# Optimization experiments

Hardware: AMD Instinct MI355X
Metric: run time of the kernel (lower is better)

The kernel has to match this reference:

```python
import jax, jax.numpy as jnp
from jax import lax
import numpy as np

N, T, PD, TD, F, E, GB = 2048, 256, 5, 5, 128, 65536, 5


def _lstm_layer(x, Wih, Whh, bih, bhh):
    # x: [B, T, D] -> [B, T, H], torch LSTM gate order (i, f, g, o)
    B = x.shape[0]
    H = Whh.shape[1]
    b = bih + bhh

    def step(carry, xt):
        h, c = carry
        gates = xt @ Wih.T + h @ Whh.T + b
        i, f, g, o = jnp.split(gates, 4, axis=-1)
        c = jax.nn.sigmoid(f) * c + jax.nn.sigmoid(i) * jnp.tanh(g)
        h = jax.nn.sigmoid(o) * jnp.tanh(c)
        return (h, c), h

    h0 = jnp.zeros((B, H), x.dtype)
    _, hs = lax.scan(step, (h0, h0), jnp.swapaxes(x, 0, 1))
    return jnp.swapaxes(hs, 0, 1)


def _attention(x, W1, b1, W2, b2):
    # Fused prefix (cumulative causal) softmax attention.
    # Original loops over t computing softmax(scores[:, :t+1]); here:
    # ctx[t] = cumsum(e * x)[t] / cumsum(e)[t] with a global max shift
    # (softmax is shift-invariant, so this equals the per-prefix softmax).
    s = (jnp.tanh(x @ W1.T + b1) @ W2.T + b2)[..., 0]  # [B, T]
    e = jnp.exp(s - jnp.max(s, axis=1, keepdims=True))  # [B, T]
    num = jnp.cumsum(e[..., None] * x, axis=1)          # [B, T, D]
    den = jnp.cumsum(e, axis=1)[..., None]              # [B, T, 1]
    return jnp.sum(num / den, axis=1)                   # [B, D]


def _gcn(x, W, b, edge_index, edge_weight):
    # PyG GCNConv with normalize=True: add self-loops (w=1), symmetric norm.
    n = x.shape[0]
    loop = jnp.arange(n)
    row = jnp.concatenate([edge_index[0], loop])
    col = jnp.concatenate([edge_index[1], loop])
    w = jnp.concatenate([edge_weight, jnp.ones((n,), edge_weight.dtype)])
    deg = jax.ops.segment_sum(w, col, num_segments=n)
    dinv = jnp.where(deg > 0, deg ** -0.5, 0.0)
    norm = dinv[row] * w * dinv[col]
    h = x @ W.T
    out = jax.ops.segment_sum(norm[:, None] * h[row], col, num_segments=n)
    return out + b


def _forward(price, global_trend, p_weights, t_weights,
             lp_Wih0, lp_Whh0, lp_bih0, lp_bhh0, lp_Wih1, lp_Whh1, lp_bih1, lp_bhh1,
             lt_Wih0, lt_Whh0, lt_bih0, lt_bhh0, lt_Wih1, lt_Whh1, lt_bih1, lt_bhh1,
             ap_W1, ap_b1, ap_W2, ap_b2, at_W1, at_b1, at_W2, at_b2,
             gp1_W, gp1_b, gp2_W, gp2_b, gt1_W, gt1_b, gt2_W, gt2_b,
             mlp_W, mlp_b, p_edge_index, t_edge_index):
    x = _lstm_layer(price, lp_Wih0, lp_Whh0, lp_bih0, lp_bhh0)
    x = _lstm_layer(x, lp_Wih1, lp_Whh1, lp_bih1, lp_bhh1)
    x = _attention(x, ap_W1, ap_b1, ap_W2, ap_b2)            # [N, F]
    g = _lstm_layer(global_trend, lt_Wih0, lt_Whh0, lt_bih0, lt_bhh0)
    g = _lstm_layer(g, lt_Wih1, lt_Whh1, lt_bih1, lt_bhh1)
    g = _attention(g, at_W1, at_b1, at_W2, at_b2)            # [GB, F]
    pg = _gcn(x, gp1_W, gp1_b, p_edge_index, p_weights)
    pg = _gcn(pg, gp2_W, gp2_b, p_edge_index, p_weights)     # [N, F]
    # NOTE: original feeds x (not g) into the trend graph convs.
    tg = _gcn(x, gt1_W, gt1_b, t_edge_index, t_weights)
    tg = _gcn(tg, gt2_W, gt2_b, t_edge_index, t_weights)     # [N, F]
    trend = tg @ g.T                                         # [N, GB]
    feat = jnp.concatenate([pg, trend], axis=1)              # [N, F+GB]
    return jax.nn.sigmoid(feat @ mlp_W.T + mlp_b)            # [N, 1]


def setup_inputs() -> dict:
    key = jax.random.key(0)
    ks = iter(jax.random.split(key, 64))
    nrm = lambda shape, s=0.05: jax.random.normal(next(ks), shape, jnp.float32) * s
    inp = {}
    inp['price'] = jax.random.normal(next(ks), (N, T, PD), jnp.float32)
    inp['global_trend'] = jax.random.normal(next(ks), (GB, T, TD), jnp.float32)
    inp['p_edge_index'] = jax.random.randint(next(ks), (2, E), 0, N)
    inp['p_weights'] = jax.random.uniform(next(ks), (E,), jnp.float32)
    inp['t_edge_index'] = jax.random.randint(next(ks), (2, E), 0, N)
    inp['t_weights'] = jax.random.uniform(next(ks), (E,), jnp.float32)
    for pre, d in (('lp', PD), ('lt', TD)):
        inp[pre + '_Wih0'] = nrm((4 * F, d)); inp[pre + '_Whh0'] = nrm((4 * F, F))
        inp[pre + '_bih0'] = nrm((4 * F,));   inp[pre + '_bhh0'] = nrm((4 * F,))
        inp[pre + '_Wih1'] = nrm((4 * F, F)); inp[pre + '_Whh1'] = nrm((4 * F, F))
        inp[pre + '_bih1'] = nrm((4 * F,));   inp[pre + '_bhh1'] = nrm((4 * F,))
    for pre in ('ap', 'at'):
        inp[pre + '_W1'] = nrm((F, F)); inp[pre + '_b1'] = jnp.zeros((F,), jnp.float32)
        inp[pre + '_W2'] = nrm((1, F)); inp[pre + '_b2'] = jnp.zeros((1,), jnp.float32)
    for pre in ('gp', 'gt'):
        inp[pre + '1_W'] = nrm((16, F)); inp[pre + '1_b'] = jnp.zeros((16,), jnp.float32)
        inp[pre + '2_W'] = nrm((F, 16)); inp[pre + '2_b'] = jnp.zeros((F,), jnp.float32)
    inp['mlp_W'] = nrm((1, F + GB)); inp['mlp_b'] = jnp.zeros((1,), jnp.float32)
    return inp


def reference(price, global_trend, p_edge_index, p_weights, t_edge_index, t_weights,
              lp_Wih0, lp_Whh0, lp_bih0, lp_bhh0, lp_Wih1, lp_Whh1, lp_bih1, lp_bhh1,
              lt_Wih0, lt_Whh0, lt_bih0, lt_bhh0, lt_Wih1, lt_Whh1, lt_bih1, lt_bhh1,
              ap_W1, ap_b1, ap_W2, ap_b2, at_W1, at_b1, at_W2, at_b2,
              gp1_W, gp1_b, gp2_W, gp2_b, gt1_W, gt1_b, gt2_W, gt2_b,
              mlp_W, mlp_b):
    return _forward(price, global_trend, p_weights, t_weights,
                    lp_Wih0, lp_Whh0, lp_bih0, lp_bhh0, lp_Wih1, lp_Whh1, lp_bih1, lp_bhh1,
                    lt_Wih0, lt_Whh0, lt_bih0, lt_bhh0, lt_Wih1, lt_Whh1, lt_bih1, lt_bhh1,
                    ap_W1, ap_b1, ap_W2, ap_b2, at_W1, at_b1, at_W2, at_b2,
                    gp1_W, gp1_b, gp2_W, gp2_b, gt1_W, gt1_b, gt2_W, gt2_b,
                    mlp_W, mlp_b, p_edge_index, t_edge_index)
```

## Files before the change

### kernel.cpp

```cpp
#include <hip/hip_runtime.h>
#include <hip/hip_bf16.h>
#include <cstddef>

#define TT    256
#define NROW  2048
#define GBN   5
#define EDG   65536

using f32x4  = __attribute__((ext_vector_type(4))) float;
using bf16x8 = __attribute__((ext_vector_type(8))) short;

__device__ __forceinline__ void pinv(bf16x8& x) { asm volatile("" : "+v"(x)); }

__device__ __forceinline__ void barrier_lgkm() {
  asm volatile("s_waitcnt lgkmcnt(0)" ::: "memory");
  __builtin_amdgcn_s_barrier();
}

__device__ __forceinline__ float exp2fa(float x) { float r; asm("v_exp_f32 %0, %1" : "=v"(r) : "v"(x)); return r; }
__device__ __forceinline__ float rcpfa(float x)  { float r; asm("v_rcp_f32 %0, %1" : "=v"(r) : "v"(x)); return r; }
#define L2E 1.4426950408889634f
__device__ __forceinline__ float sigf(float x) { return rcpfa(1.0f + exp2fa(x * -L2E)); }
__device__ __forceinline__ float tanh_fast(float x) {
  float t = exp2fa(x * (-2.0f * L2E));
  return (1.0f - t) * rcpfa(1.0f + t);
}

enum : int {
  XBUF   = 425984,
  GBUFO  = 688128,
  DINVP  = 688768,
  DINVT  = 690816,
  H16    = 692864,
  PG1    = 725632,
  H128   = 758400,
  PGB    = 1020544,
  TG1    = 1282688,
  TGB    = 1315456,
  WS_END = 1577600
};

enum : int {
  N_P0   = 0,
  N_P1I  = 65536,
  N_P1H  = 131072,
  N_PA   = 196608,
  N_T0   = 212992,
  N_T1I  = 278528,
  N_T1H  = 344064,
  N_TA   = 409600
};

enum : long long {
  C0S_O   = 1577600,
  C1S_O   = 1843840,
  H1IMG_O = 2108032,
  SMST_O  = 2372224,
  NUMS_O  = 2376352,
  ACCOS_O = 2640544,
  H0S_O   = 2904736
};

struct __align__(16) SmemPipe {
  ushort a[2][4096];
  ushort b[2][4096];
  float  x[5120];
  float  s[2][8][16];
  float  pad[8192];
};

__global__ void k_pack(const float* __restrict__ Wa, const float* __restrict__ Wb,
                       int K1, int K2, int NT, int KS, ushort* __restrict__ dst) {
  int t = blockIdx.x * blockDim.x + threadIdx.x;
  int total = KS * NT * 2 * 64;
  if (t >= total) return;
  int lane = t & 63;
  int part = (t >> 6) & 1;
  int rest = t >> 7;
  int nt = rest % NT, kk = rest / NT;
  int j = nt * 16 + (lane & 15);
  int kbase = kk * 32 + (lane >> 4) * 8;
  bf16x8 o;
  #pragma unroll
  for (int e = 0; e < 8; ++e) {
    int k = kbase + e;
    float x = (k < K1) ? Wa[(size_t)j * K1 + k] : Wb[(size_t)j * K2 + (k - K1)];
    __hip_bfloat16 hi = __float2bfloat16(x);
    ushort u;
    if (part == 0) {
      u = *(ushort*)&hi;
    } else {
      float lo = x - __bfloat162float(hi);
      __hip_bfloat16 lob = __float2bfloat16(lo);
      u = *(ushort*)&lob;
    }
    o[e] = (short)u;
  }
  ((bf16x8*)dst)[t] = o;
}

__global__ void k_zero(float* __restrict__ p, int n) {
  int i = blockIdx.x * blockDim.x + threadIdx.x;
  if (i < n) p[i] = 0.0f;
}
__global__ void k_fill1(float* __restrict__ p, int n) {
  int i = blockIdx.x * blockDim.x + threadIdx.x;
  if (i < n) p[i] = 1.0f;
}
__global__ void k_deg(const int* __restrict__ col, const float* __restrict__ w,
                      float* __restrict__ deg, int n) {
  int i = blockIdx.x * blockDim.x + threadIdx.x;
  if (i < n) atomicAdd(&deg[col[i]], w[i]);
}
__global__ void k_dinv(float* __restrict__ deg, int n) {
  int i = blockIdx.x * blockDim.x + threadIdx.x;
  if (i < n) deg[i] = rsqrtf(deg[i]);
}

__device__ static void lstm0_body(
    SmemPipe* sm, int b,
    const float* __restrict__ price, const float* __restrict__ gtrend,
    const float* __restrict__ ws_ro, ushort* __restrict__ h0S, float* __restrict__ c0S,
    const float* __restrict__ Wih0p, const float* __restrict__ bi0p, const float* __restrict__ bh0p,
    const float* __restrict__ Wih0t, const float* __restrict__ bi0t, const float* __restrict__ bh0t,
    int nP32, int t0, int TCp, int first)
{
  const int tid = threadIdx.x;
  const int w = tid >> 6, l = tid & 63;
  const int lq = l >> 4, lr = l & 15;
  const int rb = lq * 4;
  const int kcol = w * 16 + lr;
  const bool isP = b < nP32;
  const int R = isP ? 32 : GBN;
  const float* seq = isP ? (price + (size_t)b * 32 * (TT * 5)) : gtrend;
  const ushort* S0 = (const ushort*)(ws_ro + (isP ? N_P0 : N_T0));
  const float* Wih0 = isP ? Wih0p : Wih0t;
  const float* bi0 = isP ? bi0p : bi0t;
  const float* bh0 = isP ? bh0p : bh0t;

  auto h0hi = sm->a;
  auto h0lo = sm->b;
  float* xsa = sm->x;

  bf16x8 wh[4][4], wl[4][4];
  #pragma unroll
  for (int kk = 0; kk < 4; ++kk)
    #pragma unroll
    for (int g = 0; g < 4; ++g) {
      int blk = (kk * 32 + (w + 8 * g)) * 2;
      wh[kk][g] = ((const bf16x8*)S0)[(blk + 0) * 64 + l];
      wl[kk][g] = ((const bf16x8*)S0)[(blk + 1) * 64 + l];
      pinv(wh[kk][g]); pinv(wl[kk][g]);
    }
  float wih0r[4][5], bg0[4];
  #pragma unroll
  for (int g = 0; g < 4; ++g) {
    int j = kcol + 128 * g;
    bg0[g] = bi0[j] + bh0[j];
    #pragma unroll
    for (int k = 0; k < 5; ++k) wih0r[g][k] = Wih0[j * 5 + k];
  }

  const size_t bstr = (size_t)b * (size_t)TCp * 8192;
  float c0[2][4] = {{0, 0, 0, 0}, {0, 0, 0, 0}};

  for (int i = tid; i < TCp * 160; i += 512) {
    int tl = i / 160, rem = i % 160, r = rem / 5, k = rem % 5;
    xsa[tl * 160 + rem] = (r < R) ? seq[(size_t)r * (TT * 5) + (size_t)(t0 + tl) * 5 + k] : 0.0f;
  }
  if (first) {
    for (int i = tid; i < 4096; i += 512) { h0hi[0][i] = 0; h0lo[0][i] = 0; }
  } else {
    const size_t lb = bstr + (size_t)(TCp - 1) * 8192;
    *(uint4*)&h0hi[0][8 * tid] = *(const uint4*)&h0S[lb + 8 * tid];
    *(uint4*)&h0lo[0][8 * tid] = *(const uint4*)&h0S[lb + 4096 + 8 * tid];
    #pragma unroll
    for (int t = 0; t < 2; ++t)
      #pragma unroll
      for (int reg = 0; reg < 4; ++reg)
        c0[t][reg] = c0S[(size_t)b * 4096 + (size_t)(t * 16 + rb + reg) * 128 + kcol];
  }
  __syncthreads();

  const int kkhi = (kcol >> 3) & 3;
  const int eo = kcol & 7;
  const int b0w = rb + 16 * kkhi;
  const int kkw = kcol >> 5;
  int wro[4];
  #pragma unroll
  for (int reg = 0; reg < 4; ++reg) wro[reg] = kkw * 512 + (b0w + (reg ^ lq)) * 8 + eo;
  const int rdo = (l ^ ((l >> 2) & 3)) * 8;

  int cur = 0;
  for (int tl = 0; tl < TCp; ++tl) {
    const int nxt = cur ^ 1;
    if (tl > 0) {
      *(uint4*)&h0S[bstr + (size_t)(tl - 1) * 8192 + 8 * tid] = *(const uint4*)&h0hi[cur][8 * tid];
      *(uint4*)&h0S[bstr + (size_t)(tl - 1) * 8192 + 4096 + 8 * tid] = *(const uint4*)&h0lo[cur][8 * tid];
    }

    f32x4 acc[2][4];
    #pragma unroll
    for (int t = 0; t < 2; ++t)
      #pragma unroll
      for (int g = 0; g < 4; ++g) acc[t][g] = (f32x4){bg0[g], bg0[g], bg0[g], bg0[g]};
    #pragma unroll
    for (int k = 0; k < 5; ++k) {
      float xv[2][4];
      #pragma unroll
      for (int t = 0; t < 2; ++t)
        #pragma unroll
        for (int reg = 0; reg < 4; ++reg)
          xv[t][reg] = xsa[tl * 160 + (t * 16 + rb + reg) * 5 + k];
      #pragma unroll
      for (int t = 0; t < 2; ++t)
        #pragma unroll
        for (int g = 0; g < 4; ++g)
          #pragma unroll
          for (int reg = 0; reg < 4; ++reg)
            acc[t][g][reg] = fmaf(xv[t][reg], wih0r[g][k], acc[t][g][reg]);
    }
    #pragma unroll
    for (int kk = 0; kk < 4; ++kk) {
      bf16x8 ah0 = *(const bf16x8*)&h0hi[cur][kk * 512 + rdo];
      bf16x8 al0 = *(const bf16x8*)&h0lo[cur][kk * 512 + rdo];
      bf16x8 ah1 = *(const bf16x8*)&h0hi[cur][2048 + kk * 512 + rdo];
      bf16x8 al1 = *(const bf16x8*)&h0lo[cur][2048 + kk * 512 + rdo];
      #pragma unroll
      for (int g = 0; g < 4; ++g) {
        acc[0][g] = __builtin_amdgcn_mfma_f32_16x16x32_bf16(ah0, wh[kk][g], acc[0][g], 0, 0, 0);
        acc[0][g] = __builtin_amdgcn_mfma_f32_16x16x32_bf16(al0, wh[kk][g], acc[0][g], 0, 0, 0);
        acc[0][g] = __builtin_amdgcn_mfma_f32_16x16x32_bf16(ah0, wl[kk][g], acc[0][g], 0, 0, 0);
        acc[1][g] = __builtin_amdgcn_mfma_f32_16x16x32_bf16(ah1, wh[kk][g], acc[1][g], 0, 0, 0);
        acc[1][g] = __builtin_amdgcn_mfma_f32_16x16x32_bf16(al1, wh[kk][g], acc[1][g], 0, 0, 0);
        acc[1][g] = __builtin_amdgcn_mfma_f32_16x16x32_bf16(ah1, wl[kk][g], acc[1][g], 0, 0, 0);
      }
    }
    #pragma unroll
    for (int t = 0; t < 2; ++t)
      #pragma unroll
      for (int reg = 0; reg < 4; ++reg) {
        float gi = acc[0 + t][0][reg], gf = acc[t][1][reg], gg = acc[t][2][reg], go = acc[t][3][reg];
        float c = sigf(gf) * c0[t][reg] + sigf(gi) * tanh_fast(gg);
        c0[t][reg] = c;
        float h = sigf(go) * tanh_fast(c);
        __hip_bfloat16 hb = __float2bfloat16(h);
        float lo = h - __bfloat162float(hb);
        __hip_bfloat16 lb = __float2bfloat16(lo);
        h0hi[nxt][t * 2048 + wro[reg]] = *(ushort*)&hb;
        h0lo[nxt][t * 2048 + wro[reg]] = *(ushort*)&lb;
      }
    barrier_lgkm();
    cur = nxt;
  }
  *(uint4*)&h0S[bstr + (size_t)(TCp - 1) * 8192 + 8 * tid] = *(const uint4*)&h0hi[cur][8 * tid];
  *(uint4*)&h0S[bstr + (size_t)(TCp - 1) * 8192 + 4096 + 8 * tid] = *(const uint4*)&h0lo[cur][8 * tid];

  #pragma unroll
  for (int t = 0; t < 2; ++t)
    #pragma unroll
    for (int reg = 0; reg < 4; ++reg)
      c0S[(size_t)b * 4096 + (size_t)(t * 16 + rb + reg) * 128 + kcol] = c0[t][reg];
}

__device__ static void lstm1_body(
    SmemPipe* sm, int b,
    const float* __restrict__ pre1, const float* __restrict__ ws_ro,
    float* __restrict__ xout, float* __restrict__ gout,
    float* __restrict__ c1S, ushort* __restrict__ h1imgS, float* __restrict__ smS,
    float* __restrict__ numS, float* __restrict__ accOS,
    const float* __restrict__ apB1, const float* __restrict__ apW2, const float* __restrict__ apB2,
    const float* __restrict__ atB1, const float* __restrict__ atW2, const float* __restrict__ atB2,
    int nPrice, int TCp, int first)
{
  const int tid = threadIdx.x;
  const int w = tid >> 6, l = tid & 63;
  const int lq = l >> 4, lr = l & 15;
  const int rb = lq * 4;
  const int kcol = w * 16 + lr;
  const bool isP = b < nPrice;
  const int R = isP ? 16 : GBN;
  const ushort* S1H = (const ushort*)(ws_ro + (isP ? N_P1H : N_T1H));
  const ushort* SA  = (const ushort*)(ws_ro + (isP ? N_PA : N_TA));
  const float* b1ap = isP ? apB1 : atB1;
  const float* w2p  = isP ? apW2 : atW2;
  const float  b2v  = isP ? apB2[0] : atB2[0];

  auto h1hi = sm->a;
  auto h1lo = sm->b;
  auto sbuf = sm->s;

  bf16x8 hh[4][4], hl[4][4];
  #pragma unroll
  for (int kk = 0; kk < 4; ++kk)
    #pragma unroll
    for (int g = 0; g < 4; ++g) {
      int blk = (kk * 32 + (w + 8 * g)) * 2;
      hh[kk][g] = ((const bf16x8*)S1H)[(blk + 0) * 64 + l];
      hl[kk][g] = ((const bf16x8*)S1H)[(blk + 1) * 64 + l];
      pinv(hh[kk][g]); pinv(hl[kk][g]);
    }
  bf16x8 wa[4], wal[4];
  #pragma unroll
  for (int kk = 0; kk < 4; ++kk) {
    wa[kk]  = ((const bf16x8*)SA)[((kk * 8 + w) * 2 + 0) * 64 + l];
    wal[kk] = ((const bf16x8*)SA)[((kk * 8 + w) * 2 + 1) * 64 + l];
    pinv(wa[kk]); pinv(wal[kk]);
  }
  const float w2r = w2p[kcol], b1ar = b1ap[kcol];

  float c1[4] = {0, 0, 0, 0}, h1r[4] = {0, 0, 0, 0}, h1r_prev[4];
  float num[4] = {0, 0, 0, 0}, accO[4] = {0, 0, 0, 0};
  float m_run[4], den_r[4];

  if (first) {
    for (int i = tid; i < 2048; i += 512) { h1hi[0][i] = 0; h1lo[0][i] = 0; }
    #pragma unroll
    for (int reg = 0; reg < 4; ++reg) { m_run[reg] = -1e30f; den_r[reg] = 0.0f; }
  } else {
    const size_t ib = (size_t)b * 4096;
    *(uint2*)&h1hi[0][4 * tid] = *(const uint2*)&h1imgS[ib + 4 * tid];
    *(uint2*)&h1lo[0][4 * tid] = *(const uint2*)&h1imgS[ib + 2048 + 4 * tid];
    const size_t sb = (size_t)b * 2048;
    #pragma unroll
    for (int reg = 0; reg < 4; ++reg) {
      size_t o = sb + (size_t)(rb + reg) * 128 + kcol;
      c1[reg] = c1S[o];
      num[reg] = numS[o];
      accO[reg] = accOS[o];
      m_run[reg] = smS[(size_t)b * 32 + (size_t)(rb + reg) * 2];
      den_r[reg] = smS[(size_t)b * 32 + (size_t)(rb + reg) * 2 + 1];
    }
  }
  __syncthreads();

  const int kkhi = (kcol >> 3) & 3;
  const int eo = kcol & 7;
  const int b0w = rb + 16 * kkhi;
  const int kkw = kcol >> 5;
  int wro[4];
  #pragma unroll
  for (int reg = 0; reg < 4; ++reg) wro[reg] = kkw * 512 + (b0w + (reg ^ lq)) * 8 + eo;
  const int rdo = (l ^ ((l >> 2) & 3)) * 8;

  const float* pbase = pre1 + (size_t)b * TCp * 8192 + (size_t)tid * 16;

  f32x4 pnext[4];
  #pragma unroll
  for (int g = 0; g < 4; ++g) pnext[g] = *(const f32x4*)&pbase[g * 4];

  int cur = 0;
  for (int tl = 0; tl < TCp; ++tl) {
    const int nxt = cur ^ 1;
    f32x4 acc[4];
    #pragma unroll
    for (int g = 0; g < 4; ++g) acc[g] = pnext[g];
    if (tl + 1 < TCp) {
      #pragma unroll
      for (int g = 0; g < 4; ++g)
        pnext[g] = *(const f32x4*)&pbase[(size_t)(tl + 1) * 8192 + g * 4];
    }

    #pragma unroll
    for (int kk = 0; kk < 4; ++kk) {
      bf16x8 ah = *(const bf16x8*)&h1hi[cur][kk * 512 + rdo];
      bf16x8 al = *(const bf16x8*)&h1lo[cur][kk * 512 + rdo];
      #pragma unroll
      for (int g = 0; g < 4; ++g) {
        acc[g] = __builtin_amdgcn_mfma_f32_16x16x32_bf16(ah, hh[kk][g], acc[g], 0, 0, 0);
        acc[g] = __builtin_amdgcn_mfma_f32_16x16x32_bf16(al, hh[kk][g], acc[g], 0, 0, 0);
        acc[g] = __builtin_amdgcn_mfma_f32_16x16x32_bf16(ah, hl[kk][g], acc[g], 0, 0, 0);
      }
    }
    #pragma unroll
    for (int reg = 0; reg < 4; ++reg) {
      h1r_prev[reg] = h1r[reg];
      float gi = acc[0][reg], gf = acc[1][reg], gg = acc[2][reg], go = acc[3][reg];
      float c = sigf(gf) * c1[reg] + sigf(gi) * tanh_fast(gg);
      c1[reg] = c;
      float h = sigf(go) * tanh_fast(c);
      h1r[reg] = h;
      __hip_bfloat16 hb = __float2bfloat16(h);
      float lo = h - __bfloat162float(hb);
      __hip_bfloat16 lb = __float2bfloat16(lo);
      h1hi[nxt][wro[reg]] = *(ushort*)&hb;
      h1lo[nxt][wro[reg]] = *(ushort*)&lb;
    }
    barrier_lgkm();

    if (tl > 0) {
      const int pb = (tl - 1) & 1;
      #pragma unroll
      for (int reg = 0; reg < 4; ++reg) {
        float s = b2v;
        #pragma unroll
        for (int ww = 0; ww < 8; ++ww) s += sbuf[pb][ww][rb + reg];
        float m0 = m_run[reg];
        float nm = fmaxf(m0, s);
        float e = exp2fa((s - nm) * L2E), sc = exp2fa((m0 - nm) * L2E);
        float d = den_r[reg] * sc + e;
        m_run[reg] = nm; den_r[reg] = d;
        num[reg] = num[reg] * sc + e * h1r_prev[reg];
        accO[reg] = fmaf(num[reg], rcpfa(d), accO[reg]);
      }
    }

    f32x4 aa = (f32x4){b1ar, b1ar, b1ar, b1ar};
    #pragma unroll
    for (int kk = 0; kk < 4; ++kk) {
      bf16x8 ah = *(const bf16x8*)&h1hi[nxt][kk * 512 + rdo];
      bf16x8 al = *(const bf16x8*)&h1lo[nxt][kk * 512 + rdo];
      aa = __builtin_amdgcn_mfma_f32_16x16x32_bf16(ah, wa[kk], aa, 0, 0, 0);
      aa = __builtin_amdgcn_mfma_f32_16x16x32_bf16(al, wa[kk], aa, 0, 0, 0);
      aa = __builtin_amdgcn_mfma_f32_16x16x32_bf16(ah, wal[kk], aa, 0, 0, 0);
    }
    float p[4];
    #pragma unroll
    for (int reg = 0; reg < 4; ++reg) p[reg] = tanh_fast(aa[reg]) * w2r;
    #pragma unroll
    for (int m = 1; m < 16; m <<= 1) {
      #pragma unroll
      for (int reg = 0; reg < 4; ++reg) p[reg] += __shfl_xor(p[reg], m);
    }
    if (lr == 0) {
      #pragma unroll
      for (int reg = 0; reg < 4; ++reg) sbuf[tl & 1][w][rb + reg] = p[reg];
    }
    cur = nxt;
  }
  barrier_lgkm();
  {
    const int pb = (TCp - 1) & 1;
    #pragma unroll
    for (int reg = 0; reg < 4; ++reg) {
      float s = b2v;
      #pragma unroll
      for (int ww = 0; ww < 8; ++ww) s += sbuf[pb][ww][rb + reg];
      float m0 = m_run[reg];
      float nm = fmaxf(m0, s);
      float e = exp2fa((s - nm) * L2E), sc = exp2fa((m0 - nm) * L2E);
      float d = den_r[reg] * sc + e;
      m_run[reg] = nm; den_r[reg] = d;
      num[reg] = num[reg] * sc + e * h1r[reg];
      accO[reg] = fmaf(num[reg], rcpfa(d), accO[reg]);
    }
  }

  {
    const size_t ib = (size_t)b * 4096;
    *(uint2*)&h1imgS[ib + 4 * tid] = *(const uint2*)&h1hi[cur][4 * tid];
    *(uint2*)&h1imgS[ib + 2048 + 4 * tid] = *(const uint2*)&h1lo[cur][4 * tid];
    const size_t sb = (size_t)b * 2048;
    #pragma unroll
    for (int reg = 0; reg < 4; ++reg) {
      size_t o = sb + (size_t)(rb + reg) * 128 + kcol;
      c1S[o] = c1[reg];
      numS[o] = num[reg];
      accOS[o] = accO[reg];
    }
    if (w == 0 && lr == 0) {
      #pragma unroll
      for (int reg = 0; reg < 4; ++reg) {
        smS[(size_t)b * 32 + (size_t)(rb + reg) * 2] = m_run[reg];
        smS[(size_t)b * 32 + (size_t)(rb + reg) * 2 + 1] = den_r[reg];
      }
    }
  }

  float* dstx = isP ? (xout + (size_t)b * 16 * 128) : gout;
  #pragma unroll
  for (int reg = 0; reg < 4; ++reg) {
    int r = rb + reg;
    if (r < R) dstx[(size_t)r * 128 + kcol] = accO[reg];
  }
}

__global__ __launch_bounds__(512, 2) void k_pipe(
    const float* __restrict__ price, const float* __restrict__ gtrend,
    const float* __restrict__ ws_ro, ushort* __restrict__ h0S, float* __restrict__ c0S,
    const float* __restrict__ Wih0p, const float* __restrict__ bi0p, const float* __restrict__ bh0p,
    const float* __restrict__ Wih0t, const float* __restrict__ bi0t, const float* __restrict__ bh0t,
    const float* __restrict__ pre1,
    float* __restrict__ xout, float* __restrict__ gout,
    float* __restrict__ c1S, ushort* __restrict__ h1imgS, float* __restrict__ smS,
    float* __restrict__ numS, float* __restrict__ accOS,
    const float* __restrict__ apB1, const float* __restrict__ apW2, const float* __restrict__ apB2,
    const float* __restrict__ atB1, const float* __restrict__ atW2, const float* __restrict__ atB2,
    int t0A, int TCp, int firstA, int firstB, int doA, int doB)
{
  __shared__ SmemPipe sm;
  const int bid = blockIdx.x;
  if (bid < 65) {
    if (doA)
      lstm0_body(&sm, bid, price, gtrend, ws_ro, h0S, c0S,
                 Wih0p, bi0p, bh0p, Wih0t, bi0t, bh0t, 64, t0A, TCp, firstA);
  } else {
    if (doB)
      lstm1_body(&sm, bid - 65, pre1, ws_ro, xout, gout,
                 c1S, h1imgS, smS, numS, accOS,
                 apB1, apW2, apB2, atB1, atW2, atB2, 128, TCp, firstB);
  }
}

__global__ __launch_bounds__(512, 2) void k_pre1(
    const ushort* __restrict__ h0S, const float* __restrict__ ws_ro,
    float* __restrict__ pre1,
    const float* __restrict__ bi1p, const float* __restrict__ bh1p,
    const float* __restrict__ bi1t, const float* __restrict__ bh1t,
    int nPrice, int TCp, int nsub)
{
  const int b16 = blockIdx.x / nsub, sub = blockIdx.x % nsub;
  const int b32 = b16 >> 1, tile = b16 & 1;
  const int tid = threadIdx.x;
  const int w = tid >> 6, l = tid & 63;
  const int lr = l & 15;
  const int kcol = w * 16 + lr;
  const bool isP = b16 < nPrice;
  const ushort* S1I = (const ushort*)(ws_ro + (isP ? N_P1I : N_T1I));
  const float* bi1 = isP ? bi1p : bi1t;
  const float* bh1 = isP ? bh1p : bh1t;
  float bg1[4];
  #pragma unroll
  for (int g = 0; g < 4; ++g) bg1[g] = bi1[kcol + 128 * g] + bh1[kcol + 128 * g];
  const int rdo = (l ^ ((l >> 2) & 3)) * 8;
  const size_t bstr = (size_t)b32 * (size_t)TCp * 8192;
  const int t0 = sub * 4;

  f32x4 acc[4][4];
  #pragma unroll
  for (int ts = 0; ts < 4; ++ts)
    #pragma unroll
    for (int g = 0; g < 4; ++g) acc[ts][g] = (f32x4){bg1[g], bg1[g], bg1[g], bg1[g]};

  #pragma unroll
  for (int kk = 0; kk < 4; ++kk) {
    bf16x8 bh_[4], bl_[4];
    #pragma unroll
    for (int g = 0; g < 4; ++g) {
      int blk = (kk * 32 + (w + 8 * g)) * 2;
      bh_[g] = ((const bf16x8*)S1I)[(blk + 0) * 64 + l];
      bl_[g] = ((const bf16x8*)S1I)[(blk + 1) * 64 + l];
    }
    #pragma unroll
    for (int ts = 0; ts < 4; ++ts) {
      const size_t tb = bstr + (size_t)(t0 + ts) * 8192 + tile * 2048 + kk * 512 + rdo;
      bf16x8 ah = *(const bf16x8*)&h0S[tb];
      bf16x8 al = *(const bf16x8*)&h0S[tb + 4096];
      #pragma unroll
      for (int g = 0; g < 4; ++g) {
        acc[ts][g] = __builtin_amdgcn_mfma_f32_16x16x32_bf16(ah, bh_[g], acc[ts][g], 0, 0, 0);
        acc[ts][g] = __builtin_amdgcn_mfma_f32_16x16x32_bf16(al, bh_[g], acc[ts][g], 0, 0, 0);
        acc[ts][g] = __builtin_amdgcn_mfma_f32_16x16x32_bf16(ah, bl_[g], acc[ts][g], 0, 0, 0);
      }
    }
  }
  #pragma unroll
  for (int ts = 0; ts < 4; ++ts)
    #pragma unroll
    for (int g = 0; g < 4; ++g)
      *(f32x4*)&pre1[((size_t)b16 * TCp + (t0 + ts)) * 8192 + (size_t)tid * 16 + g * 4] = acc[ts][g];
}

__global__ void k_lin(const float* __restrict__ x, const float* __restrict__ W,
                      float* __restrict__ h, int M, int K, int n) {
  int i = blockIdx.x * blockDim.x + threadIdx.x;
  if (i >= n) return;
  int r = i / M, m = i % M;
  const float* xr = x + (size_t)r * K;
  const float* wm = W + (size_t)m * K;
  float a = 0.f;
  for (int k = 0; k < K; ++k) a = fmaf(xr[k], wm[k], a);
  h[i] = a;
}

__global__ void k_scatter(const int* __restrict__ rowi, const int* __restrict__ coli,
                          const float* __restrict__ w, const float* __restrict__ dinv,
                          const float* __restrict__ h, float* __restrict__ outp,
                          int M, long long n) {
  long long i = (long long)blockIdx.x * blockDim.x + threadIdx.x;
  if (i >= n) return;
  int e = (int)(i / M), f = (int)(i % M);
  int rs = rowi[e], cd = coli[e];
  float nrm = dinv[rs] * w[e] * dinv[cd];
  atomicAdd(&outp[(size_t)cd * M + f], nrm * h[(size_t)rs * M + f]);
}

__global__ void k_gcn_fin(float* __restrict__ io, const float* __restrict__ h,
                          const float* __restrict__ dinv, const float* __restrict__ b,
                          int M, int n) {
  int i = blockIdx.x * blockDim.x + threadIdx.x;
  if (i >= n) return;
  int v = i / M, f = i % M;
  float dv = dinv[v];
  io[i] += dv * dv * h[i] + b[f];
}

__global__ __launch_bounds__(256) void k_final(const float* __restrict__ pg, const float* __restrict__ tg,
                                               const float* __restrict__ g, const float* __restrict__ mw,
                                               const float* __restrict__ mb, float* __restrict__ outp) {
  int wv = threadIdx.x >> 6, ln = threadIdx.x & 63;
  int r = blockIdx.x * 4 + wv;
  const float* pr = pg + (size_t)r * 128;
  const float* tr = tg + (size_t)r * 128;
  float pa = pr[ln] * mw[ln] + pr[ln + 64] * mw[ln + 64];
  float t0 = tr[ln], t1 = tr[ln + 64];
  float s[GBN];
  #pragma unroll
  for (int gb = 0; gb < GBN; ++gb)
    s[gb] = g[gb * 128 + ln] * t0 + g[gb * 128 + 64 + ln] * t1;
  #pragma unroll
  for (int o = 32; o > 0; o >>= 1) {
    pa += __shfl_down(pa, o);
    #pragma unroll
    for (int gb = 0; gb < GBN; ++gb) s[gb] += __shfl_down(s[gb], o);
  }
  if (ln == 0) {
    float lg = pa + mb[0];
    #pragma unroll
    for (int gb = 0; gb < GBN; ++gb) lg = fmaf(s[gb], mw[128 + gb], lg);
    outp[r] = 1.0f / (1.0f + __expf(-lg));
  }
}

static inline int gdiv(long long n) { return (int)((n + 255) / 256); }

extern "C" void kernel_launch(void* const* d_in, const int* in_sizes, int n_in,
                              void* d_out, int out_size, void* d_ws, size_t ws_size,
                              hipStream_t stream) {
  const float* price  = (const float*)d_in[0];
  const float* gtrend = (const float*)d_in[1];
  const int*   p_ei   = (const int*)d_in[2];
  const float* p_w    = (const float*)d_in[3];
  const int*   t_ei   = (const int*)d_in[4];
  const float* t_w    = (const float*)d_in[5];
  const float* lpWih0 = (const float*)d_in[6];
  const float* lpWhh0 = (const float*)d_in[7];
  const float* lpBih0 = (const float*)d_in[8];
  const float* lpBhh0 = (const float*)d_in[9];
  const float* lpWih1 = (const float*)d_in[10];
  const float* lpWhh1 = (const float*)d_in[11];
  const float* lpBih1 = (const float*)d_in[12];
  const float* lpBhh1 = (const float*)d_in[13];
  const float* ltWih0 = (const float*)d_in[14];
  const float* ltWhh0 = (const float*)d_in[15];
  const float* ltBih0 = (const float*)d_in[16];
  const float* ltBhh0 = (const float*)d_in[17];
  const float* ltWih1 = (const float*)d_in[18];
  const float* ltWhh1 = (const float*)d_in[19];
  const float* ltBih1 = (const float*)d_in[20];
  const float* ltBhh1 = (const float*)d_in[21];
  const float* apW1 = (const float*)d_in[22];
  const float* apB1 = (const float*)d_in[23];
  const float* apW2 = (const float*)d_in[24];
  const float* apB2 = (const float*)d_in[25];
  const float* atW1 = (const float*)d_in[26];
  const float* atB1 = (const float*)d_in[27];
  const float* atW2 = (const float*)d_in[28];
  const float* atB2 = (const float*)d_in[29];
  const float* gp1W = (const float*)d_in[30];
  const float* gp1b = (const float*)d_in[31];
  const float* gp2W = (const float*)d_in[32];
  const float* gp2b = (const float*)d_in[33];
  const float* gt1W = (const float*)d_in[34];
  const float* gt1b = (const float*)d_in[35];
  const float* gt2W = (const float*)d_in[36];
  const float* gt2b = (const float*)d_in[37];
  const float* mlpW = (const float*)d_in[38];
  const float* mlpb = (const float*)d_in[39];

  float* ws = (float*)d_ws;
  float* outp = (float*)d_out;
  if (ws_size < (size_t)WS_END * sizeof(float)) return;

  int TC = 0;
  for (int cand = 32; cand >= 8; cand >>= 1) {
    unsigned long long need = ((unsigned long long)H0S_O +
                               65ULL * cand * 4096ULL + 129ULL * cand * 8192ULL) * 4ULL;
    if ((unsigned long long)ws_size >= need) { TC = cand; break; }
  }
  if (TC == 0) return;

  k_pack<<<gdiv(16384), 256, 0, stream>>>(lpWhh0, lpWhh0, 128, 128, 32, 4, (ushort*)(ws + N_P0));
  k_pack<<<gdiv(16384), 256, 0, stream>>>(lpWih1, lpWih1, 128, 128, 32, 4, (ushort*)(ws + N_P1I));
  k_pack<<<gdiv(16384), 256, 0, stream>>>(lpWhh1, lpWhh1, 128, 128, 32, 4, (ushort*)(ws + N_P1H));
  k_pack<<<gdiv(4096),  256, 0, stream>>>(apW1,   apW1,   128, 128,  8, 4, (ushort*)(ws + N_PA));
  k_pack<<<gdiv(16384), 256, 0, stream>>>(ltWhh0, ltWhh0, 128, 128, 32, 4, (ushort*)(ws + N_T0));
  k_pack<<<gdiv(16384), 256, 0, stream>>>(ltWih1, ltWih1, 128, 128, 32, 4, (ushort*)(ws + N_T1I));
  k_pack<<<gdiv(16384), 256, 0, stream>>>(ltWhh1, ltWhh1, 128, 128, 32, 4, (ushort*)(ws + N_T1H));
  k_pack<<<gdiv(4096),  256, 0, stream>>>(atW1,   atW1,   128, 128,  8, 4, (ushort*)(ws + N_TA));

  k_fill1<<<gdiv(NROW), 256, 0, stream>>>(ws + DINVP, NROW);
  k_deg<<<gdiv(EDG), 256, 0, stream>>>(p_ei + EDG, p_w, ws + DINVP, EDG);
  k_dinv<<<gdiv(NROW), 256, 0, stream>>>(ws + DINVP, NROW);
  k_fill1<<<gdiv(NROW), 256, 0, stream>>>(ws + DINVT, NROW);
  k_deg<<<gdiv(EDG), 256, 0, stream>>>(t_ei + EDG, t_w, ws + DINVT, EDG);
  k_dinv<<<gdiv(NROW), 256, 0, stream>>>(ws + DINVT, NROW);

  ushort* h0S = (ushort*)(ws + H0S_O);
  float*  pre1 = ws + H0S_O + (long long)65 * TC * 4096;
  {
    const int CH = TT / TC;
    const int nsub = TC / 4;
    for (int c = 0; c < CH; ++c) {
      k_pipe<<<194, 512, 0, stream>>>(price, gtrend, ws, h0S, ws + C0S_O,
                                      lpWih0, lpBih0, lpBhh0,
                                      ltWih0, ltBih0, ltBhh0,
                                      pre1, ws + XBUF, ws + GBUFO,
                                      ws + C1S_O, (ushort*)(ws + H1IMG_O), ws + SMST_O,
                                      ws + NUMS_O, ws + ACCOS_O,
                                      apB1, apW2, apB2, atB1, atW2, atB2,
                                      c * TC, TC,
                                      c == 0 ? 1 : 0, c == 1 ? 1 : 0,
                                      1, c > 0 ? 1 : 0);
      k_pre1<<<129 * nsub, 512, 0, stream>>>(h0S, ws, pre1,
                                             lpBih1, lpBhh1, ltBih1, ltBhh1,
                                             128, TC, nsub);
    }
    k_pipe<<<194, 512, 0, stream>>>(price, gtrend, ws, h0S, ws + C0S_O,
                                    lpWih0, lpBih0, lpBhh0,
                                    ltWih0, ltBih0, ltBhh0,
                                    pre1, ws + XBUF, ws + GBUFO,
                                    ws + C1S_O, (ushort*)(ws + H1IMG_O), ws + SMST_O,
                                    ws + NUMS_O, ws + ACCOS_O,
                                    apB1, apW2, apB2, atB1, atW2, atB2,
                                    0, TC, 0, CH == 1 ? 1 : 0, 0, 1);
  }

  k_lin<<<gdiv(NROW * 16), 256, 0, stream>>>(ws + XBUF, gp1W, ws + H16, 16, 128, NROW * 16);
  k_zero<<<gdiv(NROW * 16), 256, 0, stream>>>(ws + PG1, NROW * 16);
  k_scatter<<<gdiv((long long)EDG * 16), 256, 0, stream>>>(p_ei, p_ei + EDG, p_w, ws + DINVP,
                                                           ws + H16, ws + PG1, 16, (long long)EDG * 16);
  k_gcn_fin<<<gdiv(NROW * 16), 256, 0, stream>>>(ws + PG1, ws + H16, ws + DINVP, gp1b, 16, NROW * 16);
  k_lin<<<gdiv(NROW * 128), 256, 0, stream>>>(ws + PG1, gp2W, ws + H128, 128, 16, NROW * 128);
  k_zero<<<gdiv(NROW * 128), 256, 0, stream>>>(ws + PGB, NROW * 128);
  k_scatter<<<gdiv((long long)EDG * 128), 256, 0, stream>>>(p_ei, p_ei + EDG, p_w, ws + DINVP,
                                                            ws + H128, ws + PGB, 128, (long long)EDG * 128);
  k_gcn_fin<<<gdiv(NROW * 128), 256, 0, stream>>>(ws + PGB, ws + H128, ws + DINVP, gp2b, 128, NROW * 128);

  k_lin<<<gdiv(NROW * 16), 256, 0, stream>>>(ws + XBUF, gt1W, ws + H16, 16, 128, NROW * 16);
  k_zero<<<gdiv(NROW * 16), 256, 0, stream>>>(ws + TG1, NROW * 16);
  k_scatter<<<gdiv((long long)EDG * 16), 256, 0, stream>>>(t_ei, t_ei + EDG, t_w, ws + DINVT,
                                                           ws + H16, ws + TG1, 16, (long long)EDG * 16);
  k_gcn_fin<<<gdiv(NROW * 16), 256, 0, stream>>>(ws + TG1, ws + H16, ws + DINVT, gt1b, 16, NROW * 16);
  k_lin<<<gdiv(NROW * 128), 256, 0, stream>>>(ws + TG1, gt2W, ws + H128, 128, 16, NROW * 128);
  k_zero<<<gdiv(NROW * 128), 256, 0, stream>>>(ws + TGB, NROW * 128);
  k_scatter<<<gdiv((long long)EDG * 128), 256, 0, stream>>>(t_ei, t_ei + EDG, t_w, ws + DINVT,
                                                            ws + H128, ws + TGB, 128, (long long)EDG * 128);
  k_gcn_fin<<<gdiv(NROW * 128), 256, 0, stream>>>(ws + TGB, ws + H128, ws + DINVT, gt2b, 128, NROW * 128);

  k_final<<<512, 256, 0, stream>>>(ws + PGB, ws + TGB, ws + GBUFO, mlpW, mlpb, outp);
}
```

Before: 2.426 ms.

## Fuse layer-1 input projection into pipelined LSTM kernel with double-buffered h0

Removes the separate k_pre1 launch per chunk. Each layer-1 block now computes its own input projection (pre1) from the previous chunk's layer-0 hidden states at the start of k_pipe. To make this safe while layer-0 blocks write the current chunk, the h0 staging buffer is double-buffered (ping-pong hA/hB), which doubles its workspace footprint. This cuts kernel launches and lets the projection overlap with layer-0 recurrence, but it adds serial work at the front of each layer-1 block.

```diff
diff --git a/kernel.cpp b/kernel.cpp
--- a/kernel.cpp
+++ b/kernel.cpp
@@ -120,17 +120,18 @@
 __device__ static void lstm0_body(
     SmemPipe* sm, int b,
     const float* __restrict__ price, const float* __restrict__ gtrend,
-    const float* __restrict__ ws_ro, ushort* __restrict__ h0S, float* __restrict__ c0S,
+    const float* __restrict__ ws_ro, ushort* __restrict__ h0W,
+    const ushort* __restrict__ h0R, float* __restrict__ c0S,
     const float* __restrict__ Wih0p, const float* __restrict__ bi0p, const float* __restrict__ bh0p,
     const float* __restrict__ Wih0t, const float* __restrict__ bi0t, const float* __restrict__ bh0t,
-    int nP32, int t0, int TCp, int first)
+    int t0, int TCp, int first)
 {
   const int tid = threadIdx.x;
   const int w = tid >> 6, l = tid & 63;
   const int lq = l >> 4, lr = l & 15;
   const int rb = lq * 4;
   const int kcol = w * 16 + lr;
-  const bool isP = b < nP32;
+  const bool isP = b < 64;
   const int R = isP ? 32 : GBN;
   const float* seq = isP ? (price + (size_t)b * 32 * (TT * 5)) : gtrend;
   const ushort* S0 = (const ushort*)(ws_ro + (isP ? N_P0 : N_T0));
@@ -172,8 +173,8 @@
     for (int i = tid; i < 4096; i += 512) { h0hi[0][i] = 0; h0lo[0][i] = 0; }
   } else {
     const size_t lb = bstr + (size_t)(TCp - 1) * 8192;
-    *(uint4*)&h0hi[0][8 * tid] = *(const uint4*)&h0S[lb + 8 * tid];
-    *(uint4*)&h0lo[0][8 * tid] = *(const uint4*)&h0S[lb + 4096 + 8 * tid];
+    *(uint4*)&h0hi[0][8 * tid] = *(const uint4*)&h0R[lb + 8 * tid];
+    *(uint4*)&h0lo[0][8 * tid] = *(const uint4*)&h0R[lb + 4096 + 8 * tid];
     #pragma unroll
     for (int t = 0; t < 2; ++t)
       #pragma unroll
@@ -195,8 +196,8 @@
   for (int tl = 0; tl < TCp; ++tl) {
     const int nxt = cur ^ 1;
     if (tl > 0) {
-      *(uint4*)&h0S[bstr + (size_t)(tl - 1) * 8192 + 8 * tid] = *(const uint4*)&h0hi[cur][8 * tid];
-      *(uint4*)&h0S[bstr + (size_t)(tl - 1) * 8192 + 4096 + 8 * tid] = *(const uint4*)&h0lo[cur][8 * tid];
+      *(uint4*)&h0W[bstr + (size_t)(tl - 1) * 8192 + 8 * tid] = *(const uint4*)&h0hi[cur][8 * tid];
+      *(uint4*)&h0W[bstr + (size_t)(tl - 1) * 8192 + 4096 + 8 * tid] = *(const uint4*)&h0lo[cur][8 * tid];
     }
 
     f32x4 acc[2][4];
@@ -240,7 +241,7 @@
     for (int t = 0; t < 2; ++t)
       #pragma unroll
       for (int reg = 0; reg < 4; ++reg) {
-        float gi = acc[0 + t][0][reg], gf = acc[t][1][reg], gg = acc[t][2][reg], go = acc[t][3][reg];
+        float gi = acc[t][0][reg], gf = acc[t][1][reg], gg = acc[t][2][reg], go = acc[t][3][reg];
         float c = sigf(gf) * c0[t][reg] + sigf(gi) * tanh_fast(gg);
         c0[t][reg] = c;
         float h = sigf(go) * tanh_fast(c);
@@ -253,8 +254,8 @@
     barrier_lgkm();
     cur = nxt;
   }
-  *(uint4*)&h0S[bstr + (size_t)(TCp - 1) * 8192 + 8 * tid] = *(const uint4*)&h0hi[cur][8 * tid];
-  *(uint4*)&h0S[bstr + (size_t)(TCp - 1) * 8192 + 4096 + 8 * tid] = *(const uint4*)&h0lo[cur][8 * tid];
+  *(uint4*)&h0W[bstr + (size_t)(TCp - 1) * 8192 + 8 * tid] = *(const uint4*)&h0hi[cur][8 * tid];
+  *(uint4*)&h0W[bstr + (size_t)(TCp - 1) * 8192 + 4096 + 8 * tid] = *(const uint4*)&h0lo[cur][8 * tid];
 
   #pragma unroll
   for (int t = 0; t < 2; ++t)
@@ -264,24 +265,29 @@
 }
 
 __device__ static void lstm1_body(
-    SmemPipe* sm, int b,
-    const float* __restrict__ pre1, const float* __restrict__ ws_ro,
+    SmemPipe* sm, int b16,
+    const ushort* __restrict__ h0R, float* __restrict__ pre1, const float* __restrict__ ws_ro,
     float* __restrict__ xout, float* __restrict__ gout,
     float* __restrict__ c1S, ushort* __restrict__ h1imgS, float* __restrict__ smS,
     float* __restrict__ numS, float* __restrict__ accOS,
+    const float* __restrict__ bi1p, const float* __restrict__ bh1p,
     const float* __restrict__ apB1, const float* __restrict__ apW2, const float* __restrict__ apB2,
+    const float* __restrict__ bi1t, const float* __restrict__ bh1t,
     const float* __restrict__ atB1, const float* __restrict__ atW2, const float* __restrict__ atB2,
-    int nPrice, int TCp, int first)
+    int TCp, int first)
 {
   const int tid = threadIdx.x;
   const int w = tid >> 6, l = tid & 63;
   const int lq = l >> 4, lr = l & 15;
   const int rb = lq * 4;
   const int kcol = w * 16 + lr;
-  const bool isP = b < nPrice;
+  const bool isP = b16 < 128;
   const int R = isP ? 16 : GBN;
+  const ushort* S1I = (const ushort*)(ws_ro + (isP ? N_P1I : N_T1I));
   const ushort* S1H = (const ushort*)(ws_ro + (isP ? N_P1H : N_T1H));
   const ushort* SA  = (const ushort*)(ws_ro + (isP ? N_PA : N_TA));
+  const float* bi1 = isP ? bi1p : bi1t;
+  const float* bh1 = isP ? bh1p : bh1t;
   const float* b1ap = isP ? apB1 : atB1;
   const float* w2p  = isP ? apW2 : atW2;
   const float  b2v  = isP ? apB2[0] : atB2[0];
@@ -289,6 +295,52 @@
   auto h1hi = sm->a;
   auto h1lo = sm->b;
   auto sbuf = sm->s;
+
+  const int rdo = (l ^ ((l >> 2) & 3)) * 8;
+  float* pblk = pre1 + (size_t)b16 * TCp * 8192;
+
+  {
+    const int b32 = b16 >> 1, tile = b16 & 1;
+    const size_t bstr32 = (size_t)b32 * (size_t)TCp * 8192;
+    float bg1[4];
+    #pragma unroll
+    for (int g = 0; g < 4; ++g) bg1[g] = bi1[kcol + 128 * g] + bh1[kcol + 128 * g];
+    for (int g0 = 0; g0 < TCp; g0 += 2) {
+      f32x4 pacc[2][4];
+      #pragma unroll
+      for (int ts = 0; ts < 2; ++ts)
+        #pragma unroll
+        for (int g = 0; g < 4; ++g) pacc[ts][g] = (f32x4){bg1[g], bg1[g], bg1[g], bg1[g]};
+      #pragma unroll
+      for (int kk = 0; kk < 4; ++kk) {
+        bf16x8 bh_[4], bl_[4];
+        #pragma unroll
+        for (int g = 0; g < 4; ++g) {
+          int blk = (kk * 32 + (w + 8 * g)) * 2;
+          bh_[g] = ((const bf16x8*)S1I)[(blk + 0) * 64 + l];
+          bl_[g] = ((const bf16x8*)S1I)[(blk + 1) * 64 + l];
+        }
+        #pragma unroll
+        for (int ts = 0; ts < 2; ++ts) {
+          const size_t tb = bstr32 + (size_t)(g0 + ts) * 8192 + tile * 2048 + kk * 512 + rdo;
+          bf16x8 ah = *(const bf16x8*)&h0R[tb];
+          bf16x8 al = *(const bf16x8*)&h0R[tb + 4096];
+          #pragma unroll
+          for (int g = 0; g < 4; ++g) {
+            pacc[ts][g] = __builtin_amdgcn_mfma_f32_16x16x32_bf16(ah, bh_[g], pacc[ts][g], 0, 0, 0);
+            pacc[ts][g] = __builtin_amdgcn_mfma_f32_16x16x32_bf16(al, bh_[g], pacc[ts][g], 0, 0, 0);
+            pacc[ts][g] = __builtin_amdgcn_mfma_f32_16x16x32_bf16(ah, bl_[g], pacc[ts][g], 0, 0, 0);
+          }
+        }
+      }
+      #pragma unroll
+      for (int ts = 0; ts < 2; ++ts)
+        #pragma unroll
+        for (int g = 0; g < 4; ++g)
+          *(f32x4*)&pblk[(size_t)(g0 + ts) * 8192 + (size_t)tid * 16 + g * 4] = pacc[ts][g];
+    }
+    asm volatile("s_waitcnt vmcnt(0)" ::: "memory");
+  }
 
   bf16x8 hh[4][4], hl[4][4];
   #pragma unroll
@@ -318,18 +370,18 @@
     #pragma unroll
     for (int reg = 0; reg < 4; ++reg) { m_run[reg] = -1e30f; den_r[reg] = 0.0f; }
   } else {
-    const size_t ib = (size_t)b * 4096;
+    const size_t ib = (size_t)b16 * 4096;
     *(uint2*)&h1hi[0][4 * tid] = *(const uint2*)&h1imgS[ib + 4 * tid];
     *(uint2*)&h1lo[0][4 * tid] = *(const uint2*)&h1imgS[ib + 2048 + 4 * tid];
-    const size_t sb = (size_t)b * 2048;
+    const size_t sb = (size_t)b16 * 2048;
     #pragma unroll
     for (int reg = 0; reg < 4; ++reg) {
       size_t o = sb + (size_t)(rb + reg) * 128 + kcol;
       c1[reg] = c1S[o];
       num[reg] = numS[o];
       accO[reg] = accOS[o];
-      m_run[reg] = smS[(size_t)b * 32 + (size_t)(rb + reg) * 2];
-      den_r[reg] = smS[(size_t)b * 32 + (size_t)(rb + reg) * 2 + 1];
+      m_run[reg] = smS[(size_t)b16 * 32 + (size_t)(rb + reg) * 2];
+      den_r[reg] = smS[(size_t)b16 * 32 + (size_t)(rb + reg) * 2 + 1];
     }
   }
   __syncthreads();
@@ -341,9 +393,8 @@
   int wro[4];
   #pragma unroll
   for (int reg = 0; reg < 4; ++reg) wro[reg] = kkw * 512 + (b0w + (reg ^ lq)) * 8 + eo;
-  const int rdo = (l ^ ((l >> 2) & 3)) * 8;
-
-  const float* pbase = pre1 + (size_t)b * TCp * 8192 + (size_t)tid * 16;
+
+  const float* pbase = pblk + (size_t)tid * 16;
 
   f32x4 pnext[4];
   #pragma unroll
@@ -447,10 +498,10 @@
   }
 
   {
-    const size_t ib = (size_t)b * 4096;
+    const size_t ib = (size_t)b16 * 4096;
     *(uint2*)&h1imgS[ib + 4 * tid] = *(const uint2*)&h1hi[cur][4 * tid];
     *(uint2*)&h1imgS[ib + 2048 + 4 * tid] = *(const uint2*)&h1lo[cur][4 * tid];
-    const size_t sb = (size_t)b * 2048;
+    const size_t sb = (size_t)b16 * 2048;
     #pragma unroll
     for (int reg = 0; reg < 4; ++reg) {
       size_t o = sb + (size_t)(rb + reg) * 128 + kcol;
@@ -461,13 +512,13 @@
     if (w == 0 && lr == 0) {
       #pragma unroll
       for (int reg = 0; reg < 4; ++reg) {
-        smS[(size_t)b * 32 + (size_t)(rb + reg) * 2] = m_run[reg];
-        smS[(size_t)b * 32 + (size_t)(rb + reg) * 2 + 1] = den_r[reg];
+        smS[(size_t)b16 * 32 + (size_t)(rb + reg) * 2] = m_run[reg];
+        smS[(size_t)b16 * 32 + (size_t)(rb + reg) * 2 + 1] = den_r[reg];
       }
     }
   }
 
-  float* dstx = isP ? (xout + (size_t)b * 16 * 128) : gout;
+  float* dstx = isP ? (xout + (size_t)b16 * 16 * 128) : gout;
   #pragma unroll
   for (int reg = 0; reg < 4; ++reg) {
     int r = rb + reg;
@@ -477,14 +528,17 @@
 
 __global__ __launch_bounds__(512, 2) void k_pipe(
     const float* __restrict__ price, const float* __restrict__ gtrend,
-    const float* __restrict__ ws_ro, ushort* __restrict__ h0S, float* __restrict__ c0S,
+    const float* __restrict__ ws_ro, ushort* __restrict__ h0W, const ushort* __restrict__ h0R,
+    float* __restrict__ c0S,
     const float* __restrict__ Wih0p, const float* __restrict__ bi0p, const float* __restrict__ bh0p,
     const float* __restrict__ Wih0t, const float* __restrict__ bi0t, const float* __restrict__ bh0t,
-    const float* __restrict__ pre1,
+    float* __restrict__ pre1,
     float* __restrict__ xout, float* __restrict__ gout,
     float* __restrict__ c1S, ushort* __restrict__ h1imgS, float* __restrict__ smS,
     float* __restrict__ numS, float* __restrict__ accOS,
+    const float* __restrict__ bi1p, const float* __restrict__ bh1p,
     const float* __restrict__ apB1, const float* __restrict__ apW2, const float* __restrict__ apB2,
+    const float* __restrict__ bi1t, const float* __restrict__ bh1t,
     const float* __restrict__ atB1, const float* __restrict__ atW2, const float* __restrict__ atB2,
     int t0A, int TCp, int firstA, int firstB, int doA, int doB)
 {
@@ -492,73 +546,15 @@
   const int bid = blockIdx.x;
   if (bid < 65) {
     if (doA)
-      lstm0_body(&sm, bid, price, gtrend, ws_ro, h0S, c0S,
-                 Wih0p, bi0p, bh0p, Wih0t, bi0t, bh0t, 64, t0A, TCp, firstA);
+      lstm0_body(&sm, bid, price, gtrend, ws_ro, h0W, h0R, c0S,
+                 Wih0p, bi0p, bh0p, Wih0t, bi0t, bh0t, t0A, TCp, firstA);
   } else {
     if (doB)
-      lstm1_body(&sm, bid - 65, pre1, ws_ro, xout, gout,
+      lstm1_body(&sm, bid - 65, h0R, pre1, ws_ro, xout, gout,
                  c1S, h1imgS, smS, numS, accOS,
-                 apB1, apW2, apB2, atB1, atW2, atB2, 128, TCp, firstB);
-  }
-}
-
-__global__ __launch_bounds__(512, 2) void k_pre1(
-    const ushort* __restrict__ h0S, const float* __restrict__ ws_ro,
-    float* __restrict__ pre1,
-    const float* __restrict__ bi1p, const float* __restrict__ bh1p,
-    const float* __restrict__ bi1t, const float* __restrict__ bh1t,
-    int nPrice, int TCp, int nsub)
-{
-  const int b16 = blockIdx.x / nsub, sub = blockIdx.x % nsub;
-  const int b32 = b16 >> 1, tile = b16 & 1;
-  const int tid = threadIdx.x;
-  const int w = tid >> 6, l = tid & 63;
-  const int lr = l & 15;
-  const int kcol = w * 16 + lr;
-  const bool isP = b16 < nPrice;
-  const ushort* S1I = (const ushort*)(ws_ro + (isP ? N_P1I : N_T1I));
-  const float* bi1 = isP ? bi1p : bi1t;
-  const float* bh1 = isP ? bh1p : bh1t;
-  float bg1[4];
-  #pragma unroll
-  for (int g = 0; g < 4; ++g) bg1[g] = bi1[kcol + 128 * g] + bh1[kcol + 128 * g];
-  const int rdo = (l ^ ((l >> 2) & 3)) * 8;
-  const size_t bstr = (size_t)b32 * (size_t)TCp * 8192;
-  const int t0 = sub * 4;
-
-  f32x4 acc[4][4];
-  #pragma unroll
-  for (int ts = 0; ts < 4; ++ts)
-    #pragma unroll
-    for (int g = 0; g < 4; ++g) acc[ts][g] = (f32x4){bg1[g], bg1[g], bg1[g], bg1[g]};
-
-  #pragma unroll
-  for (int kk = 0; kk < 4; ++kk) {
-    bf16x8 bh_[4], bl_[4];
-    #pragma unroll
-    for (int g = 0; g < 4; ++g) {
-      int blk = (kk * 32 + (w + 8 * g)) * 2;
-      bh_[g] = ((const bf16x8*)S1I)[(blk + 0) * 64 + l];
-      bl_[g] = ((const bf16x8*)S1I)[(blk + 1) * 64 + l];
-    }
-    #pragma unroll
-    for (int ts = 0; ts < 4; ++ts) {
-      const size_t tb = bstr + (size_t)(t0 + ts) * 8192 + tile * 2048 + kk * 512 + rdo;
-      bf16x8 ah = *(const bf16x8*)&h0S[tb];
-      bf16x8 al = *(const bf16x8*)&h0S[tb + 4096];
-      #pragma unroll
-      for (int g = 0; g < 4; ++g) {
-        acc[ts][g] = __builtin_amdgcn_mfma_f32_16x16x32_bf16(ah, bh_[g], acc[ts][g], 0, 0, 0);
-        acc[ts][g] = __builtin_amdgcn_mfma_f32_16x16x32_bf16(al, bh_[g], acc[ts][g], 0, 0, 0);
-        acc[ts][g] = __builtin_amdgcn_mfma_f32_16x16x32_bf16(ah, bl_[g], acc[ts][g], 0, 0, 0);
-      }
-    }
-  }
-  #pragma unroll
-  for (int ts = 0; ts < 4; ++ts)
-    #pragma unroll
-    for (int g = 0; g < 4; ++g)
-      *(f32x4*)&pre1[((size_t)b16 * TCp + (t0 + ts)) * 8192 + (size_t)tid * 16 + g * 4] = acc[ts][g];
+                 bi1p, bh1p, apB1, apW2, apB2,
+                 bi1t, bh1t, atB1, atW2, atB2, TCp, firstB);
+  }
 }
 
 __global__ void k_lin(const float* __restrict__ x, const float* __restrict__ W,
@@ -675,7 +671,7 @@
   int TC = 0;
   for (int cand = 32; cand >= 8; cand >>= 1) {
     unsigned long long need = ((unsigned long long)H0S_O +
-                               65ULL * cand * 4096ULL + 129ULL * cand * 8192ULL) * 4ULL;
+                               2ULL * 65 * cand * 4096ULL + 129ULL * cand * 8192ULL) * 4ULL;
     if ((unsigned long long)ws_size >= need) { TC = cand; break; }
   }
   if (TC == 0) return;
@@ -696,33 +692,35 @@
   k_deg<<<gdiv(EDG), 256, 0, stream>>>(t_ei + EDG, t_w, ws + DINVT, EDG);
   k_dinv<<<gdiv(NROW), 256, 0, stream>>>(ws + DINVT, NROW);
 
-  ushort* h0S = (ushort*)(ws + H0S_O);
-  float*  pre1 = ws + H0S_O + (long long)65 * TC * 4096;
+  ushort* h0S0 = (ushort*)(ws + H0S_O);
+  ushort* h0S1 = h0S0 + (size_t)65 * TC * 8192;
+  float*  pre1 = ws + H0S_O + 2LL * 65 * TC * 4096;
   {
     const int CH = TT / TC;
-    const int nsub = TC / 4;
     for (int c = 0; c < CH; ++c) {
-      k_pipe<<<194, 512, 0, stream>>>(price, gtrend, ws, h0S, ws + C0S_O,
+      ushort* hA = (c & 1) ? h0S1 : h0S0;
+      ushort* hB = (c & 1) ? h0S0 : h0S1;
+      k_pipe<<<194, 512, 0, stream>>>(price, gtrend, ws, hA, hB, ws + C0S_O,
                                       lpWih0, lpBih0, lpBhh0,
                                       ltWih0, ltBih0, ltBhh0,
                                       pre1, ws + XBUF, ws + GBUFO,
                                       ws + C1S_O, (ushort*)(ws + H1IMG_O), ws + SMST_O,
                                       ws + NUMS_O, ws + ACCOS_O,
-                                      apB1, apW2, apB2, atB1, atW2, atB2,
+                                      lpBih1, lpBhh1, apB1, apW2, apB2,
+                                      ltBih1, ltBhh1, atB1, atW2, atB2,
                                       c * TC, TC,
                                       c == 0 ? 1 : 0, c == 1 ? 1 : 0,
                                       1, c > 0 ? 1 : 0);
-      k_pre1<<<129 * nsub, 512, 0, stream>>>(h0S, ws, pre1,
-                                             lpBih1, lpBhh1, ltBih1, ltBhh1,
-                                             128, TC, nsub);
-    }
-    k_pipe<<<194, 512, 0, stream>>>(price, gtrend, ws, h0S, ws + C0S_O,
+    }
+    ushort* hB = ((CH - 1) & 1) ? h0S1 : h0S0;
+    k_pipe<<<194, 512, 0, stream>>>(price, gtrend, ws, h0S0, hB, ws + C0S_O,
                                     lpWih0, lpBih0, lpBhh0,
                                     ltWih0, ltBih0, ltBhh0,
                                     pre1, ws + XBUF, ws + GBUFO,
                                     ws + C1S_O, (ushort*)(ws + H1IMG_O), ws + SMST_O,
                                     ws + NUMS_O, ws + ACCOS_O,
-                                    apB1, apW2, apB2, atB1, atW2, atB2,
+                                    lpBih1, lpBhh1, apB1, apW2, apB2,
+                                    ltBih1, ltBhh1, atB1, atW2, atB2,
                                     0, TC, 0, CH == 1 ? 1 : 0, 0, 1);
   }
 
```

Result: faster. 2.063 ms, median of 2 (-15.0%).
